# Kernel tuning notes

Hardware: AMD Instinct MI355X
Metric: run time of the kernel (lower is better)

The kernel has to match this reference:

```python
import jax, jax.numpy as jnp
import numpy as np

INPUT_DIM = 1024
OUTPUT_DIM = 1024
DEGREE = 8


def setup_inputs() -> dict:
    key = jax.random.key(0)
    k1, k2 = jax.random.split(key)
    x = jax.random.normal(k1, (8192, INPUT_DIM), dtype=jnp.float32)
    std = 1.0 / (INPUT_DIM * (DEGREE + 1))
    cheby_coeffs = std * jax.random.normal(k2, (INPUT_DIM, OUTPUT_DIM, DEGREE + 1), dtype=jnp.float32)
    return {"x": x, "cheby_coeffs": cheby_coeffs}


def reference(x, cheby_coeffs):
    # x: (B, I); cheby_coeffs: (I, O, D+1)
    degree = cheby_coeffs.shape[-1] - 1
    xt = jnp.tanh(x.reshape(-1, cheby_coeffs.shape[0]))
    # Chebyshev recurrence T_0=1, T_1=x, T_k = 2*x*T_{k-1} - T_{k-2}
    polys = [jnp.ones_like(xt)]
    if degree > 0:
        polys.append(xt)
    for _ in range(2, degree + 1):
        polys.append(2.0 * xt * polys[-1] - polys[-2])
    cheby = jnp.stack(polys, axis=-1)  # (B, I, D+1)
    y = jnp.einsum('bid,iod->bo', cheby, cheby_coeffs)
    return y
```

## Files before the change

kernel.cpp:

```cpp
#include <hip/hip_runtime.h>
#include <hip/hip_bf16.h>

#define AS1 __attribute__((address_space(1)))
#define AS3 __attribute__((address_space(3)))

typedef __attribute__((ext_vector_type(8))) short bf16x8;
typedef __attribute__((ext_vector_type(4))) float f32x4;

#define CSTRIDE 9216
#define KT2 8192
#define NOUT 1024

__device__ __forceinline__ void gll16(const void* g, void* l) {
    __builtin_amdgcn_global_load_lds((const AS1 void*)g, (AS3 void*)l, 16, 0, 0);
}
static __device__ __forceinline__ unsigned short f2bf(float f) {
    union { __hip_bfloat16 h; unsigned short u; } cv;
    cv.h = __float2bfloat16(f);
    return cv.u;
}
static __device__ __forceinline__ float bf2f(unsigned short u) {
    union { float f; unsigned v; } c; c.v = (unsigned)u << 16; return c.f;
}
static __device__ __forceinline__ float fast_tanhf(float v) {
    float e = __expf(2.0f * v);
    return 1.0f - 2.0f / (e + 1.0f);
}

__global__ void __launch_bounds__(256) prep_kernel(const float* __restrict__ cc,
                                                   unsigned short* __restrict__ Wt,
                                                   float* __restrict__ bias) {
    __shared__ unsigned short T[288 * 68];
    const int t  = threadIdx.x;
    const int n0 = (blockIdx.x & 31) * 32;
    const int i0 = (blockIdx.x >> 5) * 64;

    for (int il = 0; il < 64; ++il) {
        const float* src = cc + (size_t)(i0 + il) * CSTRIDE + (size_t)n0 * 9;
        for (int f = t; f < 288; f += 256)
            T[f * 68 + il] = f2bf(src[f]);
    }
    __syncthreads();

#pragma unroll
    for (int it = 0; it < 16; ++it) {
        const int chunk = it * 16 + (t >> 4);
        const int nl = chunk >> 3;
        const int dd = chunk & 7;
        const int n  = n0 + nl;
        const int e0 = (t & 15) * 4;
        const int isrc = e0 ^ ((n & 7) << 3);
        ushort4 v = *(const ushort4*)&T[(nl * 9 + dd + 1) * 68 + isrc];
        *(ushort4*)(Wt + (size_t)n * KT2 + dd * 1024 + i0 + e0) = v;
    }

    if (t < 32) {
        float s = 0.f;
#pragma unroll 8
        for (int il = 0; il < 64; ++il) s += bf2f(T[(t * 9) * 68 + il]);
        atomicAdd(&bias[n0 + t], s);
    }
}

__global__ void __launch_bounds__(512, 4)
cheby_gemm(const float* __restrict__ x, const unsigned short* __restrict__ Wt,
           const float* __restrict__ bias, float* __restrict__ out) {
    __shared__ unsigned short Asub[128 * 64];
    __shared__ unsigned short Bsub[128 * 64];

    const int id   = blockIdx.x;
    const int bcol = (id & 7) * 128;
    const int brow = (id >> 3) * 128;
    const int t    = threadIdx.x;
    const int lane = t & 63;
    const int w    = t >> 6;
    const int wr   = (w >> 2) * 64;
    const int wc   = (w & 3) * 32;
    const int l15  = lane & 15;
    const int lhi  = lane >> 4;

    const int gi0 = (t & 15) * 4;
    const int gr  = t >> 4;
    const int bl3 = (lane >> 3);
    const int bp8 = (lane & 7) * 8;

    unsigned awoff[4];
#pragma unroll
    for (int p = 0; p < 4; ++p) {
        const int r = gr + 32 * p;
        awoff[p] = r * 128 + ((gi0 * 2) ^ ((r & 7) << 4));
    }

    f32x4 acc[4][2] = {};
    float x2[4][4], Tp[4][4], Tpp[4][4];

#pragma unroll 1
    for (int ic = 0; ic < 16; ++ic) {
#pragma unroll
        for (int dd = 0; dd < 8; ++dd) {
            __syncthreads();

            const int kb = dd * 1024 + ic * 64;
#pragma unroll
            for (int c = 0; c < 2; ++c) {
                const int n_loc = w * 16 + c * 8 + bl3;
                gll16(Wt + (size_t)(bcol + n_loc) * KT2 + kb + bp8,
                      (char*)Bsub + (w * 16 + c * 8) * 128);
            }

            if (dd == 0) {
#pragma unroll
                for (int p = 0; p < 4; ++p) {
                    const float4 v = *(const float4*)(x +
                        (size_t)(brow + gr + 32 * p) * 1024 + ic * 64 + gi0);
                    ushort4 pk; unsigned short* pks = (unsigned short*)&pk;
#pragma unroll
                    for (int j = 0; j < 4; ++j) {
                        x2[p][j] = 2.0f * fast_tanhf((&v.x)[j]);
                        const float c = 0.5f * x2[p][j];
                        Tp[p][j] = c; Tpp[p][j] = 1.0f;
                        pks[j] = f2bf(c);
                    }
                    *(ushort4*)((char*)Asub + awoff[p]) = pk;
                }
            } else {
#pragma unroll
                for (int p = 0; p < 4; ++p) {
                    ushort4 pk; unsigned short* pks = (unsigned short*)&pk;
#pragma unroll
                    for (int j = 0; j < 4; ++j) {
                        const float c = __builtin_fmaf(x2[p][j], Tp[p][j], -Tpp[p][j]);
                        Tpp[p][j] = Tp[p][j]; Tp[p][j] = c;
                        pks[j] = f2bf(c);
                    }
                    *(ushort4*)((char*)Asub + awoff[p]) = pk;
                }
            }

            __syncthreads();

#pragma unroll
            for (int ks = 0; ks < 2; ++ks) {
                bf16x8 af[4], bfr[2];
#pragma unroll
                for (int mf = 0; mf < 4; ++mf) {
                    const int row = wr + mf * 16 + l15;
                    af[mf] = *(const bf16x8*)((const char*)Asub + row * 128 +
                              ((ks * 64 + lhi * 16) ^ ((row & 7) << 4)));
                }
#pragma unroll
                for (int nf = 0; nf < 2; ++nf) {
                    const int n = wc + nf * 16 + l15;
                    bfr[nf] = *(const bf16x8*)((const char*)Bsub + n * 128 +
                              ((ks * 64 + lhi * 16) ^ ((n & 7) << 4)));
                }
#pragma unroll
                for (int mf = 0; mf < 4; ++mf)
#pragma unroll
                    for (int nf = 0; nf < 2; ++nf)
                        acc[mf][nf] = __builtin_amdgcn_mfma_f32_16x16x32_bf16(
                            af[mf], bfr[nf], acc[mf][nf], 0, 0, 0);
            }
        }
    }

    float bv[2];
#pragma unroll
    for (int nf = 0; nf < 2; ++nf) bv[nf] = bias[bcol + wc + nf * 16 + l15];
#pragma unroll
    for (int mf = 0; mf < 4; ++mf)
#pragma unroll
        for (int nf = 0; nf < 2; ++nf)
#pragma unroll
            for (int ri = 0; ri < 4; ++ri) {
                const int orow = brow + wr + mf * 16 + lhi * 4 + ri;
                const int ocol = bcol + wc + nf * 16 + l15;
                out[(size_t)orow * NOUT + ocol] = acc[mf][nf][ri] + bv[nf];
            }
}

__global__ void __launch_bounds__(256) naive_kernel(const float* __restrict__ x,
                                                    const float* __restrict__ cc,
                                                    float* __restrict__ out) {
    __shared__ float xs[1024];
    const int b = blockIdx.x;
    const int t = threadIdx.x;
#pragma unroll
    for (int j = 0; j < 4; ++j)
        xs[t * 4 + j] = fast_tanhf(x[(size_t)b * 1024 + t * 4 + j]);
    __syncthreads();

    const int o = t * 4;
    float a0 = 0.f, a1 = 0.f, a2 = 0.f, a3 = 0.f;
    for (int i = 0; i < 1024; ++i) {
        const float* cp = cc + (size_t)i * CSTRIDE + (size_t)o * 9;
        const float xv = xs[i];
        float tpp = 1.0f, tp = xv;
        a0 += cp[0];  a1 += cp[9];  a2 += cp[18];  a3 += cp[27];
        a0 += xv * cp[1]; a1 += xv * cp[10]; a2 += xv * cp[19]; a3 += xv * cp[28];
#pragma unroll
        for (int d = 2; d <= 8; ++d) {
            const float cur = 2.0f * xv * tp - tpp;
            tpp = tp; tp = cur;
            a0 += cur * cp[d];      a1 += cur * cp[9 + d];
            a2 += cur * cp[18 + d]; a3 += cur * cp[27 + d];
        }
    }
    float* op = out + (size_t)b * NOUT + o;
    op[0] = a0; op[1] = a1; op[2] = a2; op[3] = a3;
}

extern "C" void kernel_launch(void* const* d_in, const int* in_sizes, int n_in,
                              void* d_out, int out_size, void* d_ws, size_t ws_size,
                              hipStream_t stream) {
    const float* x  = (const float*)d_in[0];
    const float* cc = (const float*)d_in[1];
    float* out = (float*)d_out;

    const size_t wt_bytes = (size_t)KT2 * 1024 * sizeof(unsigned short);
    const size_t need = wt_bytes + 1024 * sizeof(float);
    if (ws_size >= need) {
        unsigned short* Wt = (unsigned short*)d_ws;
        float* bias = (float*)((char*)d_ws + wt_bytes);
        hipMemsetAsync(bias, 0, 1024 * sizeof(float), stream);
        prep_kernel<<<512, 256, 0, stream>>>(cc, Wt, bias);
        cheby_gemm<<<512, 512, 0, stream>>>(x, Wt, bias, out);
    } else {
        naive_kernel<<<8192, 256, 0, stream>>>(x, cc, out);
    }
}
```

Measured before the change: 240.0 us.

## Double-buffer LDS tiles to overlap next-step loads with MFMA compute

Splits the A and B shared-memory tiles into two buffers. While the current step's fragments are read and fed to MFMA, the next step's weight tile is fetched and the next Chebyshev A tile is generated into the other buffer. This cuts the two barriers per k-step down to one and hides global-load latency. In exchange LDS use per block doubles to 64KB, which may reduce occupancy below the four blocks per CU that the launch bounds request.

```diff
diff --git a/kernel.cpp b/kernel.cpp
--- a/kernel.cpp
+++ b/kernel.cpp
@@ -65,8 +65,8 @@
 __global__ void __launch_bounds__(512, 4)
 cheby_gemm(const float* __restrict__ x, const unsigned short* __restrict__ Wt,
            const float* __restrict__ bias, float* __restrict__ out) {
-    __shared__ unsigned short Asub[128 * 64];
-    __shared__ unsigned short Bsub[128 * 64];
+    __shared__ unsigned short Asub[2][128 * 64];
+    __shared__ unsigned short Bsub[2][128 * 64];
 
     const int id   = blockIdx.x;
     const int bcol = (id & 7) * 128;
@@ -84,6 +84,9 @@
     const int bl3 = (lane >> 3);
     const int bp8 = (lane & 7) * 8;
 
+    char* const Abase = (char*)&Asub[0][0];
+    char* const Bbase = (char*)&Bsub[0][0];
+
     unsigned awoff[4];
 #pragma unroll
     for (int p = 0; p < 4; ++p) {
@@ -94,73 +97,106 @@
     f32x4 acc[4][2] = {};
     float x2[4][4], Tp[4][4], Tpp[4][4];
 
+#pragma unroll
+    for (int c = 0; c < 2; ++c) {
+        const int n_loc = w * 16 + c * 8;
+        gll16(Wt + (size_t)(bcol + n_loc + bl3) * KT2 + bp8,
+              Bbase + n_loc * 128);
+    }
+#pragma unroll
+    for (int p = 0; p < 4; ++p) {
+        const float4 v = *(const float4*)(x + (size_t)(brow + gr + 32 * p) * 1024 + gi0);
+        ushort4 pk; unsigned short* pks = (unsigned short*)&pk;
+#pragma unroll
+        for (int j = 0; j < 4; ++j) {
+            x2[p][j] = 2.0f * fast_tanhf((&v.x)[j]);
+            const float c = 0.5f * x2[p][j];
+            Tp[p][j] = c; Tpp[p][j] = 1.0f;
+            pks[j] = f2bf(c);
+        }
+        *(ushort4*)(Abase + awoff[p]) = pk;
+    }
+    __syncthreads();
+
 #pragma unroll 1
     for (int ic = 0; ic < 16; ++ic) {
 #pragma unroll
         for (int dd = 0; dd < 8; ++dd) {
-            __syncthreads();
-
-            const int kb = dd * 1024 + ic * 64;
-#pragma unroll
-            for (int c = 0; c < 2; ++c) {
-                const int n_loc = w * 16 + c * 8 + bl3;
-                gll16(Wt + (size_t)(bcol + n_loc) * KT2 + kb + bp8,
-                      (char*)Bsub + (w * 16 + c * 8) * 128);
-            }
-
-            if (dd == 0) {
-#pragma unroll
-                for (int p = 0; p < 4; ++p) {
-                    const float4 v = *(const float4*)(x +
-                        (size_t)(brow + gr + 32 * p) * 1024 + ic * 64 + gi0);
-                    ushort4 pk; unsigned short* pks = (unsigned short*)&pk;
-#pragma unroll
-                    for (int j = 0; j < 4; ++j) {
-                        x2[p][j] = 2.0f * fast_tanhf((&v.x)[j]);
-                        const float c = 0.5f * x2[p][j];
-                        Tp[p][j] = c; Tpp[p][j] = 1.0f;
-                        pks[j] = f2bf(c);
-                    }
-                    *(ushort4*)((char*)Asub + awoff[p]) = pk;
-                }
-            } else {
-#pragma unroll
-                for (int p = 0; p < 4; ++p) {
-                    ushort4 pk; unsigned short* pks = (unsigned short*)&pk;
-#pragma unroll
-                    for (int j = 0; j < 4; ++j) {
-                        const float c = __builtin_fmaf(x2[p][j], Tp[p][j], -Tpp[p][j]);
-                        Tpp[p][j] = Tp[p][j]; Tp[p][j] = c;
-                        pks[j] = f2bf(c);
-                    }
-                    *(ushort4*)((char*)Asub + awoff[p]) = pk;
-                }
-            }
-
-            __syncthreads();
-
+            const int s    = ic * 8 + dd;
+            const int curo = (s & 1) << 14;
+            const int nxto = curo ^ 16384;
+            const bool pre = (s != 127);
+            const int ddn  = (dd + 1) & 7;
+            const int icn  = (dd == 7) ? (ic + 1) : ic;
+
+            if (pre) {
+                const int kbn = ddn * 1024 + icn * 64;
+#pragma unroll
+                for (int c = 0; c < 2; ++c) {
+                    const int n_loc = w * 16 + c * 8;
+                    gll16(Wt + (size_t)(bcol + n_loc + bl3) * KT2 + kbn + bp8,
+                          Bbase + nxto + n_loc * 128);
+                }
+            }
+
+            bf16x8 af[2][4], bfr[2][2];
 #pragma unroll
             for (int ks = 0; ks < 2; ++ks) {
-                bf16x8 af[4], bfr[2];
 #pragma unroll
                 for (int mf = 0; mf < 4; ++mf) {
                     const int row = wr + mf * 16 + l15;
-                    af[mf] = *(const bf16x8*)((const char*)Asub + row * 128 +
-                              ((ks * 64 + lhi * 16) ^ ((row & 7) << 4)));
+                    af[ks][mf] = *(const bf16x8*)(Abase + curo + row * 128 +
+                                  ((ks * 64 + lhi * 16) ^ ((row & 7) << 4)));
                 }
 #pragma unroll
                 for (int nf = 0; nf < 2; ++nf) {
                     const int n = wc + nf * 16 + l15;
-                    bfr[nf] = *(const bf16x8*)((const char*)Bsub + n * 128 +
-                              ((ks * 64 + lhi * 16) ^ ((n & 7) << 4)));
-                }
+                    bfr[ks][nf] = *(const bf16x8*)(Bbase + curo + n * 128 +
+                                  ((ks * 64 + lhi * 16) ^ ((n & 7) << 4)));
+                }
+            }
+
+            if (pre) {
+                if (ddn == 0) {
+#pragma unroll
+                    for (int p = 0; p < 4; ++p) {
+                        const float4 v = *(const float4*)(x +
+                            (size_t)(brow + gr + 32 * p) * 1024 + icn * 64 + gi0);
+                        ushort4 pk; unsigned short* pks = (unsigned short*)&pk;
+#pragma unroll
+                        for (int j = 0; j < 4; ++j) {
+                            x2[p][j] = 2.0f * fast_tanhf((&v.x)[j]);
+                            const float c = 0.5f * x2[p][j];
+                            Tp[p][j] = c; Tpp[p][j] = 1.0f;
+                            pks[j] = f2bf(c);
+                        }
+                        *(ushort4*)(Abase + nxto + awoff[p]) = pk;
+                    }
+                } else {
+#pragma unroll
+                    for (int p = 0; p < 4; ++p) {
+                        ushort4 pk; unsigned short* pks = (unsigned short*)&pk;
+#pragma unroll
+                        for (int j = 0; j < 4; ++j) {
+                            const float c = __builtin_fmaf(x2[p][j], Tp[p][j], -Tpp[p][j]);
+                            Tpp[p][j] = Tp[p][j]; Tp[p][j] = c;
+                            pks[j] = f2bf(c);
+                        }
+                        *(ushort4*)(Abase + nxto + awoff[p]) = pk;
+                    }
+                }
+            }
+
+#pragma unroll
+            for (int ks = 0; ks < 2; ++ks)
 #pragma unroll
                 for (int mf = 0; mf < 4; ++mf)
 #pragma unroll
                     for (int nf = 0; nf < 2; ++nf)
                         acc[mf][nf] = __builtin_amdgcn_mfma_f32_16x16x32_bf16(
-                            af[mf], bfr[nf], acc[mf][nf], 0, 0, 0);
-            }
+                            af[ks][mf], bfr[ks][nf], acc[mf][nf], 0, 0, 0);
+
+            __syncthreads();
         }
     }
 
```

Result: slower. 377.6 us (+57.4%).
